# Optimization experiments

Measured on AMD Instinct MI355X. Metric: run time of the kernel, lower is better.

## Reference

```python
import jax, jax.numpy as jnp
import numpy as np

SEQ = 16384
HID = 1280
HEADS = 16
HEAD_DIM = HID // HEADS  # 80
NUM_WIN = 16
WIN = SEQ // NUM_WIN  # 1024


def rotate_half(x):
    x1, x2 = jnp.split(x, 2, axis=-1)
    return jnp.concatenate([-x2, x1], axis=-1)


def setup_inputs() -> dict:
    key = jax.random.key(0)
    ks = jax.random.split(key, 8)
    pos = jnp.arange(SEQ, dtype=jnp.float32)[:, None]
    inv_freq = 1.0 / (10000.0 ** (jnp.arange(0, HEAD_DIM, 2, dtype=jnp.float32) / HEAD_DIM))
    ang = pos * inv_freq[None, :]
    ang = jnp.concatenate([ang, ang], axis=-1)  # [SEQ, HEAD_DIM]
    return {
        "hidden_states": jax.random.normal(ks[0], (SEQ, HID), dtype=jnp.float32),
        "cos": jnp.cos(ang),
        "sin": jnp.sin(ang),
        "qkv_kernel": jax.random.normal(ks[1], (HID, 3 * HID), dtype=jnp.float32) * 0.02,
        "qkv_bias": jnp.zeros((3 * HID,), dtype=jnp.float32),
        "proj_kernel": jax.random.normal(ks[2], (HID, HID), dtype=jnp.float32) * 0.02,
        "proj_bias": jnp.zeros((HID,), dtype=jnp.float32),
        "cu_seqlens": jnp.arange(NUM_WIN + 1, dtype=jnp.int32) * WIN,
    }


def reference(hidden_states, cos, sin, qkv_kernel, qkv_bias, proj_kernel, proj_bias, cu_seqlens):
    seq_len = hidden_states.shape[0]
    scale = HEAD_DIM ** (-0.5)
    qkv = hidden_states @ qkv_kernel + qkv_bias
    q, k, v = jnp.split(qkv, 3, axis=-1)
    q = q.reshape(seq_len, HEADS, HEAD_DIM)
    k = k.reshape(seq_len, HEADS, HEAD_DIM)
    v = v.reshape(seq_len, HEADS, HEAD_DIM)
    c = cos[:, None, :HEAD_DIM]
    s = sin[:, None, :HEAD_DIM]
    q = q * c + rotate_half(q) * s
    k = k * c + rotate_half(k) * s
    num_win = cu_seqlens.shape[0] - 1
    win = seq_len // num_win
    qw = q.reshape(num_win, win, HEADS, HEAD_DIM).astype(jnp.float32)
    kw = k.reshape(num_win, win, HEADS, HEAD_DIM).astype(jnp.float32)
    vw = v.reshape(num_win, win, HEADS, HEAD_DIM).astype(jnp.float32)
    scores = jnp.einsum('wqhd,wkhd->whqk', qw, kw) * scale
    weights = jax.nn.softmax(scores, axis=-1)
    out = jnp.einsum('whqk,wkhd->wqhd', weights, vw)
    out = out.reshape(seq_len, HID)
    return out @ proj_kernel + proj_bias
```

## Files before the change

### kernel.cpp

```cpp
#include <hip/hip_runtime.h>
#include <stdint.h>

#define SEQ 16384
#define HIDN 1280
#define NHEADS 16
#define HD 80
#define HDP 96
#define NWIN 16
#define WINSZ 1024

typedef unsigned short u16;
typedef unsigned int u32;
typedef __bf16 bf16x8 __attribute__((ext_vector_type(8)));
typedef float f32x4 __attribute__((ext_vector_type(4)));

#define AS1 __attribute__((address_space(1)))
#define AS3 __attribute__((address_space(3)))

__device__ __forceinline__ u16 f2b(float f) {
  __bf16 h = (__bf16)f;
  return __builtin_bit_cast(u16, h);
}
__device__ __forceinline__ u32 f2b2(float lo, float hi) {
  __bf16 l = (__bf16)lo, h = (__bf16)hi;
  return (u32)__builtin_bit_cast(u16, l) | ((u32)__builtin_bit_cast(u16, h) << 16);
}
__device__ __forceinline__ float b2f(u16 u) { return __uint_as_float(((u32)u) << 16); }

__device__ __forceinline__ float fexp2(float x) {
#if __has_builtin(__builtin_amdgcn_exp2f)
  return __builtin_amdgcn_exp2f(x);
#else
  return exp2f(x);
#endif
}

__device__ __forceinline__ void load_lds16(const void* g, void* l) {
  __builtin_amdgcn_global_load_lds((AS1 void*)g, (AS3 void*)l, 16, 0, 0);
}

__global__ void k_cvt(const float* __restrict__ in, u16* __restrict__ out) {
  size_t i = ((size_t)blockIdx.x * 256 + threadIdx.x) * 4;
  float4 v = *(const float4*)(in + i);
  uint2 o;
  o.x = f2b2(v.x, v.y);
  o.y = f2b2(v.z, v.w);
  *(uint2*)(out + i) = o;
}

__global__ void k_trans(const float* __restrict__ in, u16* __restrict__ out, int R, int C) {
  __shared__ float tile[64][65];
  int c0 = blockIdx.x * 64, r0 = blockIdx.y * 64;
  int tc = threadIdx.x & 63, tr4 = threadIdx.x >> 6;
#pragma unroll
  for (int i = 0; i < 16; i++) {
    int r = tr4 + i * 4;
    tile[r][tc] = in[(size_t)(r0 + r) * C + c0 + tc];
  }
  __syncthreads();
#pragma unroll
  for (int i = 0; i < 16; i++) {
    int r = tr4 + i * 4;
    out[(size_t)(c0 + r) * R + r0 + tc] = f2b(tile[tc][r]);
  }
}


#define GBAR() asm volatile("s_barrier" ::: "memory")

template <int MODE>
__launch_bounds__(512, 2)
__global__ void k_gemm8(const u16* __restrict__ A, const u16* __restrict__ B,
                        const float* __restrict__ bias, float* __restrict__ outf,
                        u16* __restrict__ Qb, u16* __restrict__ Kb, u16* __restrict__ Vt,
                        int N, int ncol) {
  extern __shared__ char lds[];
  const int K = 1280;
  const int NT = 40;
  const int tid = threadIdx.x;
  const int wv = tid >> 6, lane = tid & 63;
  const int lr = lane & 15, lq = lane >> 4;
  const int wm = wv >> 2, wn = wv & 3;
  const int id = blockIdx.x;
  const int xs = id & 7, rest = id >> 3;
  const int cb = rest % ncol, rs = rest / ncol;
  const int row0 = (rs * 8 + xs) * 256, col0 = cb * 256;

  const u16* gA[2];
  const u16* gB[2];
  int Pst[2];
#pragma unroll
  for (int ld = 0; ld < 2; ld++) {
    int P = wv * 2048 + ld * 1024 + lane * 16;
    int j = P >> 7;
    int Wl = (P & 127) ^ ((j & 7) << 4);
    int r = 2 * j + (Wl >> 6);
    int c = (Wl & 63) >> 1;
    gA[ld] = A + (size_t)(row0 + r) * K + c;
    gB[ld] = B + (size_t)(col0 + r) * K + c;
    Pst[ld] = P;
  }

  int offA[2][4], offB[4];
#pragma unroll
  for (int ch = 0; ch < 2; ch++)
#pragma unroll
    for (int a = 0; a < 4; a++) {
      int r = wm * 128 + ch * 64 + a * 16 + lr;
      int j = r >> 1;
      int Wl = ((r & 1) << 6) | (lq << 4);
      offA[ch][a] = j * 128 + (Wl ^ ((j & 7) << 4));
    }
#pragma unroll
  for (int ni = 0; ni < 4; ni++) {
    int r = wn * 64 + ni * 16 + lr;
    int j = r >> 1;
    int Wl = ((r & 1) << 6) | (lq << 4);
    offB[ni] = 16384 + j * 128 + (Wl ^ ((j & 7) << 4));
  }

  f32x4 acc[8][4];
#pragma unroll
  for (int i = 0; i < 8; i++)
#pragma unroll
    for (int j = 0; j < 4; j++) acc[i][j] = (f32x4){0.f, 0.f, 0.f, 0.f};

#define STAGE(mat_, kt_)                                             \
  do {                                                               \
    char* lb_ = lds + (((kt_) & 3) << 15) + ((mat_) << 14);          \
    const u16* g0_ = (mat_) ? gB[0] : gA[0];                         \
    const u16* g1_ = (mat_) ? gB[1] : gA[1];                         \
    int ko_ = (kt_) * 32;                                            \
    load_lds16(g0_ + ko_, lb_ + Pst[0]);                             \
    load_lds16(g1_ + ko_, lb_ + Pst[1]);                             \
  } while (0)

#define MFMA16(dst_, af_, bf_)                                               \
  do {                                                                       \
    __builtin_amdgcn_s_setprio(1);                                           \
    _Pragma("unroll") for (int a_ = 0; a_ < 4; a_++)                         \
        _Pragma("unroll") for (int n_ = 0; n_ < 4; n_++)                     \
            acc[dst_ + a_][n_] = __builtin_amdgcn_mfma_f32_16x16x32_bf16(    \
                af_[a_], bf_[n_], acc[dst_ + a_][n_], 0, 0, 0);              \
    __builtin_amdgcn_s_setprio(0);                                           \
  } while (0)

  STAGE(0, 0);
  STAGE(1, 0);
  STAGE(0, 1);
  STAGE(1, 1);
  STAGE(0, 2);
  STAGE(1, 2);
  asm volatile("s_waitcnt vmcnt(8)" ::: "memory");
  GBAR();

#pragma unroll 4
  for (int t = 0; t < NT; t++) {
    const int bb = (t & 3) << 15;
    bf16x8 bfr[4], af0[4], af1[4];

#pragma unroll
    for (int ni = 0; ni < 4; ni++) bfr[ni] = *(const bf16x8*)(lds + bb + offB[ni]);
#pragma unroll
    for (int a = 0; a < 4; a++) af0[a] = *(const bf16x8*)(lds + bb + offA[0][a]);
    if (t + 3 < NT) STAGE(0, t + 3);
    GBAR();
    MFMA16(0, af0, bfr);
    GBAR();

#pragma unroll
    for (int a = 0; a < 4; a++) af1[a] = *(const bf16x8*)(lds + bb + offA[1][a]);
    if (t + 3 < NT) STAGE(1, t + 3);
    if (t + 3 < NT)
      asm volatile("s_waitcnt vmcnt(8)" ::: "memory");
    else if (t == NT - 3)
      asm volatile("s_waitcnt vmcnt(4)" ::: "memory");
    else if (t == NT - 2)
      asm volatile("s_waitcnt vmcnt(0)" ::: "memory");
    GBAR();
    MFMA16(4, af1, bfr);
    GBAR();
  }
#undef STAGE
#undef MFMA16

#pragma unroll
  for (int ni = 0; ni < 4; ni++) {
    int col = col0 + wn * 64 + ni * 16 + lr;
    float bs = bias[col];
    if (MODE == 0) {
#pragma unroll
      for (int mi = 0; mi < 8; mi++)
#pragma unroll
        for (int r = 0; r < 4; r++) {
          int row = row0 + wm * 128 + mi * 16 + lq * 4 + r;
          outf[(size_t)row * N + col] = acc[mi][ni][r] + bs;
        }
    } else {
      int seg = col / HIDN;
      int cl = col - seg * HIDN;
      int h = cl / HD, d = cl - h * HD;
      if (seg == 2) {
#pragma unroll
        for (int mi = 0; mi < 8; mi++) {
          int row = row0 + wm * 128 + mi * 16 + lq * 4;
          uint2 o;
          o.x = f2b2(acc[mi][ni][0] + bs, acc[mi][ni][1] + bs);
          o.y = f2b2(acc[mi][ni][2] + bs, acc[mi][ni][3] + bs);
          *(uint2*)(Vt + ((size_t)h * HD + d) * SEQ + row) = o;
        }
      } else {
        u16* Dst = (seg == 0) ? Qb : Kb;
#pragma unroll
        for (int mi = 0; mi < 8; mi++)
#pragma unroll
          for (int r = 0; r < 4; r++) {
            int row = row0 + wm * 128 + mi * 16 + lq * 4 + r;
            Dst[((size_t)h * SEQ + row) * HDP + d] = f2b(acc[mi][ni][r] + bs);
          }
      }
    }
  }
}

__global__ void k_rope2(u16* __restrict__ Q, u16* __restrict__ K,
                        const float* __restrict__ cs, const float* __restrict__ sn) {
  int idx = blockIdx.x * 256 + threadIdx.x;
  const int TOT = NHEADS * SEQ * 10;
  u16* X = Q;
  if (idx >= TOT) { X = K; idx -= TOT; }
  int h = idx / (SEQ * 10);
  int rem = idx - h * (SEQ * 10);
  int s = rem / 10;
  int t = rem - s * 10;
  int d = t * 4;
  size_t base = ((size_t)h * SEQ + s) * HDP;
  float4 cv = *(const float4*)(cs + s * HD + d);
  float4 sv = *(const float4*)(sn + s * HD + d);
  uint2 a = *(const uint2*)(X + base + d);
  uint2 b = *(const uint2*)(X + base + d + 40);
  float x1[4], x2[4];
  x1[0] = b2f(a.x & 0xffffu); x1[1] = b2f(a.x >> 16);
  x1[2] = b2f(a.y & 0xffffu); x1[3] = b2f(a.y >> 16);
  x2[0] = b2f(b.x & 0xffffu); x2[1] = b2f(b.x >> 16);
  x2[2] = b2f(b.y & 0xffffu); x2[3] = b2f(b.y >> 16);
  uint2 o1, o2;
  o1.x = f2b2(x1[0] * cv.x - x2[0] * sv.x, x1[1] * cv.y - x2[1] * sv.y);
  o1.y = f2b2(x1[2] * cv.z - x2[2] * sv.z, x1[3] * cv.w - x2[3] * sv.w);
  o2.x = f2b2(x2[0] * cv.x + x1[0] * sv.x, x2[1] * cv.y + x1[1] * sv.y);
  o2.y = f2b2(x2[2] * cv.z + x1[2] * sv.z, x2[3] * cv.w + x1[3] * sv.w);
  *(uint2*)(X + base + d) = o1;
  *(uint2*)(X + base + d + 40) = o2;
  if (t < 4) {
    uint2 z; z.x = 0; z.y = 0;
    *(uint2*)(X + base + 80 + t * 4) = z;
  }
}

__launch_bounds__(256, 2)
__global__ void k_attn(const u16* __restrict__ Qb, const u16* __restrict__ Kb,
                       const u16* __restrict__ Vt, u16* __restrict__ Ob) {
  __shared__ char lds[24576 + 20480 + 4 * 4352];
  char* ldsK = lds;
  char* ldsV = lds + 24576;
  char* ldsP = lds + 45056;

  const int tid = threadIdx.x;
  const int wv = tid >> 6, lane = tid & 63;
  const int lr = lane & 15, lq = lane >> 4;

  const int b = blockIdx.x;
  const int qblk = b & 7, h = (b >> 3) & 15, w = b >> 7;
  const int q0 = w * WINSZ + qblk * 128 + wv * 32;
  const int kwin = w * WINSZ;

  bf16x8 qf[2][3];
#pragma unroll
  for (int qt = 0; qt < 2; qt++)
#pragma unroll
    for (int ds = 0; ds < 3; ds++)
      qf[qt][ds] = *(const bf16x8*)(Qb + ((size_t)h * SEQ + q0 + qt * 16 + lr) * HDP + ds * 32 + lq * 8);

  f32x4 acc[2][5];
#pragma unroll
  for (int i = 0; i < 2; i++)
#pragma unroll
    for (int j = 0; j < 5; j++) acc[i][j] = (f32x4){0.f, 0.f, 0.f, 0.f};
  float mo[2] = {-1e30f, -1e30f};
  float lsum[2] = {0.f, 0.f};
  const float kscale = 0.11180339887498949f * 1.4426950408889634f;

  for (int kt = 0; kt < 8; kt++) {
    int k0 = kwin + kt * 128;
#pragma unroll
    for (int li = 0; li < 11; li++) {
      int g = li * 4 + wv;
      const u16* gp;
      char* lp;
      if (g < 24) {
        int kt16 = g / 3, ds = g - kt16 * 3;
        gp = Kb + ((size_t)h * SEQ + k0 + kt16 * 16 + lr) * HDP + ds * 32 + lq * 8;
        lp = ldsK + g * 1024;
      } else {
        int g2 = g - 24;
        int dt = g2 >> 2, ks = g2 & 3;
        gp = Vt + ((size_t)h * HD + dt * 16 + lr) * SEQ + k0 + ks * 32 + lq * 8;
        lp = ldsV + g2 * 1024;
      }
      load_lds16(gp, lp);
    }
    __syncthreads();

    f32x4 sx[2][8];
#pragma unroll
    for (int i = 0; i < 2; i++)
#pragma unroll
      for (int j = 0; j < 8; j++) sx[i][j] = (f32x4){0.f, 0.f, 0.f, 0.f};
    __builtin_amdgcn_s_setprio(1);
#pragma unroll
    for (int kt16 = 0; kt16 < 8; kt16++) {
      bf16x8 kf0 = *(const bf16x8*)(ldsK + (kt16 * 3 + 0) * 1024 + lane * 16);
      bf16x8 kf1 = *(const bf16x8*)(ldsK + (kt16 * 3 + 1) * 1024 + lane * 16);
      bf16x8 kf2 = *(const bf16x8*)(ldsK + (kt16 * 3 + 2) * 1024 + lane * 16);
#pragma unroll
      for (int qt = 0; qt < 2; qt++) {
        sx[qt][kt16] = __builtin_amdgcn_mfma_f32_16x16x32_bf16(kf0, qf[qt][0], sx[qt][kt16], 0, 0, 0);
        sx[qt][kt16] = __builtin_amdgcn_mfma_f32_16x16x32_bf16(kf1, qf[qt][1], sx[qt][kt16], 0, 0, 0);
        sx[qt][kt16] = __builtin_amdgcn_mfma_f32_16x16x32_bf16(kf2, qf[qt][2], sx[qt][kt16], 0, 0, 0);
      }
    }
    __builtin_amdgcn_s_setprio(0);

    bf16x8 pf[2][4];
#pragma unroll
    for (int qt = 0; qt < 2; qt++) {
      float mx = -1e30f;
#pragma unroll
      for (int t = 0; t < 8; t++)
#pragma unroll
        for (int r = 0; r < 4; r++) mx = fmaxf(mx, sx[qt][t][r]);
      mx = fmaxf(mx, __shfl_xor(mx, 16));
      mx = fmaxf(mx, __shfl_xor(mx, 32));
      float mxs = mx * kscale;
      if (!__all(mxs <= mo[qt] + 8.f)) {
        float mnew = fmaxf(mo[qt], mxs);
        float alpha = fexp2(mo[qt] - mnew);
        mo[qt] = mnew;
        lsum[qt] *= alpha;
#pragma unroll
        for (int dt = 0; dt < 5; dt++) acc[qt][dt] *= alpha;
      }
      float ls = 0.f;
#pragma unroll
      for (int t = 0; t < 8; t++)
#pragma unroll
        for (int r = 0; r < 4; r++) {
          float p = fexp2(fmaf(sx[qt][t][r], kscale, -mo[qt]));
          sx[qt][t][r] = p;
          ls += p;
        }
      ls += __shfl_xor(ls, 16);
      ls += __shfl_xor(ls, 32);
      lsum[qt] += ls;
      char* pw = ldsP + wv * 4352;
#pragma unroll
      for (int t = 0; t < 8; t++) {
        uint2 o;
        o.x = f2b2(sx[qt][t][0], sx[qt][t][1]);
        o.y = f2b2(sx[qt][t][2], sx[qt][t][3]);
        *(uint2*)(pw + lr * 272 + t * 32 + lq * 8) = o;
      }
#pragma unroll
      for (int ks = 0; ks < 4; ks++)
        pf[qt][ks] = *(const bf16x8*)(pw + lr * 272 + ks * 64 + lq * 16);
    }

    __builtin_amdgcn_s_setprio(1);
#pragma unroll
    for (int dt = 0; dt < 5; dt++)
#pragma unroll
      for (int ks = 0; ks < 4; ks++) {
        bf16x8 vf = *(const bf16x8*)(ldsV + (dt * 4 + ks) * 1024 + lane * 16);
#pragma unroll
        for (int qt = 0; qt < 2; qt++)
          acc[qt][dt] = __builtin_amdgcn_mfma_f32_16x16x32_bf16(vf, pf[qt][ks], acc[qt][dt], 0, 0, 0);
      }
    __builtin_amdgcn_s_setprio(0);
    __syncthreads();
  }

#pragma unroll
  for (int qt = 0; qt < 2; qt++) {
    float rl = 1.f / lsum[qt];
    int s = q0 + qt * 16 + lr;
#pragma unroll
    for (int dt = 0; dt < 5; dt++) {
      uint2 o;
      o.x = f2b2(acc[qt][dt][0] * rl, acc[qt][dt][1] * rl);
      o.y = f2b2(acc[qt][dt][2] * rl, acc[qt][dt][3] * rl);
      size_t ob = (size_t)s * HIDN + h * HD + dt * 16 + lq * 4;
      *(uint2*)(Ob + ob) = o;
    }
  }
}

extern "C" void kernel_launch(void* const* d_in, const int* in_sizes, int n_in,
                              void* d_out, int out_size, void* d_ws, size_t ws_size,
                              hipStream_t stream) {
  (void)in_sizes; (void)n_in; (void)out_size; (void)ws_size;
  const float* hidden = (const float*)d_in[0];
  const float* cosb   = (const float*)d_in[1];
  const float* sinb   = (const float*)d_in[2];
  const float* qkvk   = (const float*)d_in[3];
  const float* qkvb   = (const float*)d_in[4];
  const float* projk  = (const float*)d_in[5];
  const float* projb  = (const float*)d_in[6];

  char* ws = (char*)d_ws;
  u16* Abf = (u16*)(ws + 0);
  u16* Wt  = (u16*)(ws + 41943040);
  u16* Pt  = (u16*)(ws + 51773440);
  u16* Qb  = (u16*)(ws + 55050240);
  u16* Kb  = (u16*)(ws + 105381888);
  u16* Vtb = (u16*)(ws + 155713536);

  static int attr_done = 0;
  if (!attr_done) {
    (void)hipFuncSetAttribute((const void*)&k_gemm8<1>,
                              hipFuncAttributeMaxDynamicSharedMemorySize, 131072);
    (void)hipFuncSetAttribute((const void*)&k_gemm8<0>,
                              hipFuncAttributeMaxDynamicSharedMemorySize, 131072);
    (void)hipGetLastError();
    attr_done = 1;
  }

  k_cvt<<<20480, 256, 0, stream>>>(hidden, Abf);
  k_trans<<<dim3(60, 20), 256, 0, stream>>>(qkvk, Wt, 1280, 3840);
  k_trans<<<dim3(20, 20), 256, 0, stream>>>(projk, Pt, 1280, 1280);
  k_gemm8<1><<<960, 512, 131072, stream>>>(Abf, Wt, qkvb, nullptr, Qb, Kb, Vtb, 3840, 15);
  k_rope2<<<20480, 256, 0, stream>>>(Qb, Kb, cosb, sinb);
  k_attn<<<2048, 256, 0, stream>>>(Qb, Kb, Vtb, Abf);
  k_gemm8<0><<<320, 512, 131072, stream>>>(Abf, Pt, projb, (float*)d_out,
                                           nullptr, nullptr, nullptr, 1280, 5);
}
```

Baseline: 618.9 us.

## Load GEMM B-operand and attention V fragments directly from global memory

```diff
diff --git a/kernel.cpp b/kernel.cpp
--- a/kernel.cpp
+++ b/kernel.cpp
@@ -13,6 +13,7 @@
 typedef unsigned int u32;
 typedef __bf16 bf16x8 __attribute__((ext_vector_type(8)));
 typedef float f32x4 __attribute__((ext_vector_type(4)));
+typedef u32 u32x4 __attribute__((ext_vector_type(4)));
 
 #define AS1 __attribute__((address_space(1)))
 #define AS3 __attribute__((address_space(3)))
@@ -38,6 +39,8 @@
 __device__ __forceinline__ void load_lds16(const void* g, void* l) {
   __builtin_amdgcn_global_load_lds((AS1 void*)g, (AS3 void*)l, 16, 0, 0);
 }
+
+#define GBAR() asm volatile("s_barrier" ::: "memory")
 
 __global__ void k_cvt(const float* __restrict__ in, u16* __restrict__ out) {
   size_t i = ((size_t)blockIdx.x * 256 + threadIdx.x) * 4;
@@ -65,13 +68,16 @@
   }
 }
 
-
-#define GBAR() asm volatile("s_barrier" ::: "memory")
-
-template <int MODE>
+__device__ __forceinline__ void waitv_t(int t) {
+  if (t <= 36) asm volatile("s_waitcnt vmcnt(8)" ::: "memory");
+  else if (t == 37) asm volatile("s_waitcnt vmcnt(6)" ::: "memory");
+  else if (t == 38) asm volatile("s_waitcnt vmcnt(4)" ::: "memory");
+  else asm volatile("s_waitcnt vmcnt(0)" ::: "memory");
+}
+
 __launch_bounds__(512, 2)
-__global__ void k_gemm8(const u16* __restrict__ A, const u16* __restrict__ B,
-                        const float* __restrict__ bias, float* __restrict__ outf,
+__global__ void k_gemmB(const u16* __restrict__ A, const u16* __restrict__ B,
+                        const float* __restrict__ bias,
                         u16* __restrict__ Qb, u16* __restrict__ Kb, u16* __restrict__ Vt,
                         int N, int ncol) {
   extern __shared__ char lds[];
@@ -87,6 +93,160 @@
   const int row0 = (rs * 8 + xs) * 256, col0 = cb * 256;
 
   const u16* gA[2];
+  int Pst[2];
+#pragma unroll
+  for (int ld = 0; ld < 2; ld++) {
+    int P = wv * 2048 + ld * 1024 + lane * 16;
+    int j = P >> 7;
+    int Wl = (P & 127) ^ ((j & 7) << 4);
+    int r = 2 * j + (Wl >> 6);
+    int c = (Wl & 63) >> 1;
+    gA[ld] = A + (size_t)(row0 + r) * K + c;
+    Pst[ld] = P;
+  }
+
+  int offA[2][4];
+#pragma unroll
+  for (int ch = 0; ch < 2; ch++)
+#pragma unroll
+    for (int a = 0; a < 4; a++) {
+      int r = wm * 128 + ch * 64 + a * 16 + lr;
+      int j = r >> 1;
+      int Wl = ((r & 1) << 6) | (lq << 4);
+      offA[ch][a] = j * 128 + (Wl ^ ((j & 7) << 4));
+    }
+
+  const u16* gBp[4];
+#pragma unroll
+  for (int ni = 0; ni < 4; ni++)
+    gBp[ni] = B + (size_t)(col0 + wn * 64 + ni * 16 + lr) * K + lq * 8;
+
+  f32x4 acc[8][4];
+#pragma unroll
+  for (int i = 0; i < 8; i++)
+#pragma unroll
+    for (int j = 0; j < 4; j++) acc[i][j] = (f32x4){0.f, 0.f, 0.f, 0.f};
+
+#define STAGEA(kt_)                                                  \
+  do {                                                               \
+    char* lb_ = lds + (((kt_) & 3) << 14);                           \
+    int ko_ = (kt_) * 32;                                            \
+    load_lds16(gA[0] + ko_, lb_ + Pst[0]);                           \
+    load_lds16(gA[1] + ko_, lb_ + Pst[1]);                           \
+  } while (0)
+
+#define LOADB(dst_)                                                  \
+  do {                                                               \
+    _Pragma("unroll") for (int ni = 0; ni < 4; ni++) {               \
+      u32x4 tmp_;                                                    \
+      asm volatile("global_load_dwordx4 %0, %1, off"                 \
+                   : "=v"(tmp_) : "v"(gBp[ni]));                     \
+      dst_[ni] = __builtin_bit_cast(bf16x8, tmp_);                   \
+      gBp[ni] += 32;                                                 \
+    }                                                                \
+  } while (0)
+
+#define MFMA16(dst_, af_, bf_)                                               \
+  do {                                                                       \
+    __builtin_amdgcn_s_setprio(1);                                           \
+    _Pragma("unroll") for (int a_ = 0; a_ < 4; a_++)                         \
+        _Pragma("unroll") for (int n_ = 0; n_ < 4; n_++)                     \
+            acc[dst_ + a_][n_] = __builtin_amdgcn_mfma_f32_16x16x32_bf16(    \
+                af_[a_], bf_[n_], acc[dst_ + a_][n_], 0, 0, 0);              \
+    __builtin_amdgcn_s_setprio(0);                                           \
+  } while (0)
+
+  bf16x8 bP[4], bQ[4];
+  STAGEA(0);
+  STAGEA(1);
+  STAGEA(2);
+  LOADB(bP);
+  asm volatile("s_waitcnt vmcnt(0)" ::: "memory");
+  GBAR();
+
+  for (int t = 0; t < NT; t += 2) {
+    {
+      const int bb = (t & 3) << 14;
+      bf16x8 af0[4], af1[4];
+#pragma unroll
+      for (int a = 0; a < 4; a++) af0[a] = *(const bf16x8*)(lds + bb + offA[0][a]);
+#pragma unroll
+      for (int a = 0; a < 4; a++) af1[a] = *(const bf16x8*)(lds + bb + offA[1][a]);
+      LOADB(bQ);
+      if (t + 3 < NT) STAGEA(t + 3);
+      waitv_t(t);
+      __builtin_amdgcn_sched_barrier(0);
+      MFMA16(0, af0, bP);
+      MFMA16(4, af1, bP);
+      GBAR();
+    }
+    {
+      const int tt = t + 1;
+      const int bb = (tt & 3) << 14;
+      bf16x8 af0[4], af1[4];
+#pragma unroll
+      for (int a = 0; a < 4; a++) af0[a] = *(const bf16x8*)(lds + bb + offA[0][a]);
+#pragma unroll
+      for (int a = 0; a < 4; a++) af1[a] = *(const bf16x8*)(lds + bb + offA[1][a]);
+      if (tt + 1 < NT) LOADB(bP);
+      if (tt + 3 < NT) STAGEA(tt + 3);
+      waitv_t(tt);
+      __builtin_amdgcn_sched_barrier(0);
+      MFMA16(0, af0, bQ);
+      MFMA16(4, af1, bQ);
+      GBAR();
+    }
+  }
+#undef STAGEA
+#undef LOADB
+#undef MFMA16
+
+#pragma unroll
+  for (int ni = 0; ni < 4; ni++) {
+    int col = col0 + wn * 64 + ni * 16 + lr;
+    float bs = bias[col];
+    int seg = col / HIDN;
+    int cl = col - seg * HIDN;
+    int h = cl / HD, d = cl - h * HD;
+    if (seg == 2) {
+#pragma unroll
+      for (int mi = 0; mi < 8; mi++) {
+        int row = row0 + wm * 128 + mi * 16 + lq * 4;
+        uint2 o;
+        o.x = f2b2(acc[mi][ni][0] + bs, acc[mi][ni][1] + bs);
+        o.y = f2b2(acc[mi][ni][2] + bs, acc[mi][ni][3] + bs);
+        *(uint2*)(Vt + ((size_t)h * HD + d) * SEQ + row) = o;
+      }
+    } else {
+      u16* Dst = (seg == 0) ? Qb : Kb;
+#pragma unroll
+      for (int mi = 0; mi < 8; mi++)
+#pragma unroll
+        for (int r = 0; r < 4; r++) {
+          int row = row0 + wm * 128 + mi * 16 + lq * 4 + r;
+          Dst[((size_t)h * SEQ + row) * HDP + d] = f2b(acc[mi][ni][r] + bs);
+        }
+    }
+  }
+}
+
+__launch_bounds__(512, 2)
+__global__ void k_gemmL(const u16* __restrict__ A, const u16* __restrict__ B,
+                        const float* __restrict__ bias, float* __restrict__ outf,
+                        int N, int ncol) {
+  extern __shared__ char lds[];
+  const int K = 1280;
+  const int NT = 40;
+  const int tid = threadIdx.x;
+  const int wv = tid >> 6, lane = tid & 63;
+  const int lr = lane & 15, lq = lane >> 4;
+  const int wm = wv >> 2, wn = wv & 3;
+  const int id = blockIdx.x;
+  const int xs = id & 7, rest = id >> 3;
+  const int cb = rest % ncol, rs = rest / ncol;
+  const int row0 = (rs * 8 + xs) * 256, col0 = cb * 256;
+
+  const u16* gA[2];
   const u16* gB[2];
   int Pst[2];
 #pragma unroll
@@ -135,7 +295,7 @@
     load_lds16(g1_ + ko_, lb_ + Pst[1]);                             \
   } while (0)
 
-#define MFMA16(dst_, af_, bf_)                                               \
+#define MFMA16L(dst_, af_, bf_)                                              \
   do {                                                                       \
     __builtin_amdgcn_s_setprio(1);                                           \
     _Pragma("unroll") for (int a_ = 0; a_ < 4; a_++)                         \
@@ -158,19 +318,16 @@
   for (int t = 0; t < NT; t++) {
     const int bb = (t & 3) << 15;
     bf16x8 bfr[4], af0[4], af1[4];
-
 #pragma unroll
     for (int ni = 0; ni < 4; ni++) bfr[ni] = *(const bf16x8*)(lds + bb + offB[ni]);
 #pragma unroll
     for (int a = 0; a < 4; a++) af0[a] = *(const bf16x8*)(lds + bb + offA[0][a]);
     if (t + 3 < NT) STAGE(0, t + 3);
-    GBAR();
-    MFMA16(0, af0, bfr);
-    GBAR();
-
+    MFMA16L(0, af0, bfr);
 #pragma unroll
     for (int a = 0; a < 4; a++) af1[a] = *(const bf16x8*)(lds + bb + offA[1][a]);
     if (t + 3 < NT) STAGE(1, t + 3);
+    MFMA16L(4, af1, bfr);
     if (t + 3 < NT)
       asm volatile("s_waitcnt vmcnt(8)" ::: "memory");
     else if (t == NT - 3)
@@ -178,48 +335,21 @@
     else if (t == NT - 2)
       asm volatile("s_waitcnt vmcnt(0)" ::: "memory");
     GBAR();
-    MFMA16(4, af1, bfr);
-    GBAR();
   }
 #undef STAGE
-#undef MFMA16
+#undef MFMA16L
 
 #pragma unroll
   for (int ni = 0; ni < 4; ni++) {
     int col = col0 + wn * 64 + ni * 16 + lr;
     float bs = bias[col];
-    if (MODE == 0) {
-#pragma unroll
-      for (int mi = 0; mi < 8; mi++)
-#pragma unroll
-        for (int r = 0; r < 4; r++) {
-          int row = row0 + wm * 128 + mi * 16 + lq * 4 + r;
-          outf[(size_t)row * N + col] = acc[mi][ni][r] + bs;
-        }
-    } else {
-      int seg = col / HIDN;
-      int cl = col - seg * HIDN;
-      int h = cl / HD, d = cl - h * HD;
-      if (seg == 2) {
-#pragma unroll
-        for (int mi = 0; mi < 8; mi++) {
-          int row = row0 + wm * 128 + mi * 16 + lq * 4;
-          uint2 o;
-          o.x = f2b2(acc[mi][ni][0] + bs, acc[mi][ni][1] + bs);
-          o.y = f2b2(acc[mi][ni][2] + bs, acc[mi][ni][3] + bs);
-          *(uint2*)(Vt + ((size_t)h * HD + d) * SEQ + row) = o;
-        }
-      } else {
-        u16* Dst = (seg == 0) ? Qb : Kb;
-#pragma unroll
-        for (int mi = 0; mi < 8; mi++)
-#pragma unroll
-          for (int r = 0; r < 4; r++) {
-            int row = row0 + wm * 128 + mi * 16 + lq * 4 + r;
-            Dst[((size_t)h * SEQ + row) * HDP + d] = f2b(acc[mi][ni][r] + bs);
-          }
+#pragma unroll
+    for (int mi = 0; mi < 8; mi++)
+#pragma unroll
+      for (int r = 0; r < 4; r++) {
+        int row = row0 + wm * 128 + mi * 16 + lq * 4 + r;
+        outf[(size_t)row * N + col] = acc[mi][ni][r] + bs;
       }
-    }
   }
 }
 
@@ -260,10 +390,9 @@
 __launch_bounds__(256, 2)
 __global__ void k_attn(const u16* __restrict__ Qb, const u16* __restrict__ Kb,
                        const u16* __restrict__ Vt, u16* __restrict__ Ob) {
-  __shared__ char lds[24576 + 20480 + 4 * 4352];
+  __shared__ char lds[24576 + 4 * 4352];
   char* ldsK = lds;
-  char* ldsV = lds + 24576;
-  char* ldsP = lds + 45056;
+  char* ldsP = lds + 24576;
 
   const int tid = threadIdx.x;
   const int wv = tid >> 6, lane = tid & 63;
@@ -281,6 +410,8 @@
     for (int ds = 0; ds < 3; ds++)
       qf[qt][ds] = *(const bf16x8*)(Qb + ((size_t)h * SEQ + q0 + qt * 16 + lr) * HDP + ds * 32 + lq * 8);
 
+  const u16* vb = Vt + ((size_t)h * HD + lr) * SEQ + lq * 8;
+
   f32x4 acc[2][5];
 #pragma unroll
   for (int i = 0; i < 2; i++)
@@ -293,21 +424,11 @@
   for (int kt = 0; kt < 8; kt++) {
     int k0 = kwin + kt * 128;
 #pragma unroll
-    for (int li = 0; li < 11; li++) {
+    for (int li = 0; li < 6; li++) {
       int g = li * 4 + wv;
-      const u16* gp;
-      char* lp;
-      if (g < 24) {
-        int kt16 = g / 3, ds = g - kt16 * 3;
-        gp = Kb + ((size_t)h * SEQ + k0 + kt16 * 16 + lr) * HDP + ds * 32 + lq * 8;
-        lp = ldsK + g * 1024;
-      } else {
-        int g2 = g - 24;
-        int dt = g2 >> 2, ks = g2 & 3;
-        gp = Vt + ((size_t)h * HD + dt * 16 + lr) * SEQ + k0 + ks * 32 + lq * 8;
-        lp = ldsV + g2 * 1024;
-      }
-      load_lds16(gp, lp);
+      int kt16 = g / 3, ds = g - kt16 * 3;
+      const u16* gp = Kb + ((size_t)h * SEQ + k0 + kt16 * 16 + lr) * HDP + ds * 32 + lq * 8;
+      load_lds16(gp, ldsK + g * 1024);
     }
     __syncthreads();
 
@@ -380,7 +501,7 @@
     for (int dt = 0; dt < 5; dt++)
 #pragma unroll
       for (int ks = 0; ks < 4; ks++) {
-        bf16x8 vf = *(const bf16x8*)(ldsV + (dt * 4 + ks) * 1024 + lane * 16);
+        bf16x8 vf = *(const bf16x8*)(vb + (size_t)(dt * 16) * SEQ + k0 + ks * 32);
 #pragma unroll
         for (int qt = 0; qt < 2; qt++)
           acc[qt][dt] = __builtin_amdgcn_mfma_f32_16x16x32_bf16(vf, pf[qt][ks], acc[qt][dt], 0, 0, 0);
@@ -426,9 +547,9 @@
 
   static int attr_done = 0;
   if (!attr_done) {
-    (void)hipFuncSetAttribute((const void*)&k_gemm8<1>,
-                              hipFuncAttributeMaxDynamicSharedMemorySize, 131072);
-    (void)hipFuncSetAttribute((const void*)&k_gemm8<0>,
+    (void)hipFuncSetAttribute((const void*)&k_gemmB,
+                              hipFuncAttributeMaxDynamicSharedMemorySize, 65536);
+    (void)hipFuncSetAttribute((const void*)&k_gemmL,
                               hipFuncAttributeMaxDynamicSharedMemorySize, 131072);
     (void)hipGetLastError();
     attr_done = 1;
@@ -437,9 +558,8 @@
   k_cvt<<<20480, 256, 0, stream>>>(hidden, Abf);
   k_trans<<<dim3(60, 20), 256, 0, stream>>>(qkvk, Wt, 1280, 3840);
   k_trans<<<dim3(20, 20), 256, 0, stream>>>(projk, Pt, 1280, 1280);
-  k_gemm8<1><<<960, 512, 131072, stream>>>(Abf, Wt, qkvb, nullptr, Qb, Kb, Vtb, 3840, 15);
+  k_gemmB<<<960, 512, 65536, stream>>>(Abf, Wt, qkvb, Qb, Kb, Vtb, 3840, 15);
   k_rope2<<<20480, 256, 0, stream>>>(Qb, Kb, cosb, sinb);
   k_attn<<<2048, 256, 0, stream>>>(Qb, Kb, Vtb, Abf);
-  k_gemm8<0><<<320, 512, 131072, stream>>>(Abf, Pt, projb, (float*)d_out,
-                                           nullptr, nullptr, nullptr, 1280, 5);
-}
+  k_gemmL<<<320, 512, 131072, stream>>>(Abf, Pt, projb, (float*)d_out, 1280, 5);
+}
```

Result: slower. 763.8 us (+23.4%).
